# Optimization experiments

Hardware: AMD Instinct MI355X
Metric: run time of the kernel (lower is better)

The kernel has to match this reference:

```python
import jax, jax.numpy as jnp
import numpy as np

BLOCK = 8
INDICES_RADIUS = 127.0  # radius of int8 index dtype


def _dct_matrix(n: int) -> np.ndarray:
    """Orthonormal DCT-II matrix M[element, frequency] matching transforms.cosine."""
    e = np.arange(n)[:, None].astype(np.float64)
    f = np.arange(n)[None, :].astype(np.float64)
    m = np.sqrt(2.0 / n) * np.cos(np.pi * (2.0 * e + 1.0) * f / (2.0 * n))
    m[:, 0] = np.sqrt(1.0 / n)
    return m.astype(np.float32)


def setup_inputs() -> dict:
    key = jax.random.key(0)
    x = jax.random.normal(key, (8192, 8192), dtype=jnp.float32)
    dct = jnp.asarray(_dct_matrix(BLOCK))
    return {"x": x, "dct": dct}


def reference(x, dct):
    # Block splitting: blocked[b1,b2,e1,e2] = x[8*b1+e1, 8*b2+e2]
    H, W = x.shape  # already multiples of BLOCK, so padding is a no-op
    b1, b2 = H // BLOCK, W // BLOCK
    blocked = x.reshape(b1, BLOCK, b2, BLOCK).transpose(0, 2, 1, 3)  # (b1,b2,8,8)
    # Separable blockwise DCT: contract intra-block axes with M[element,freq]
    coeffs = jnp.einsum("bcef,eg,fh->bcgh", blocked, dct, dct)
    # mask is all-ones 8x8 -> row-major flatten of intra-block coefficients
    flat = coeffs.reshape(b1, b2, BLOCK * BLOCK)  # (b1,b2,64)
    # bin(): per-block inf-norm then uniform quantization to int8 bins
    biggest = jnp.max(jnp.abs(flat), axis=-1)  # (b1,b2)
    indices = jnp.round(flat * (INDICES_RADIUS / biggest[..., None])).astype(jnp.int8)
    return indices, biggest
```

## Files before the change

### kernel.cpp

```cpp
#include <hip/hip_runtime.h>


#define IMG_H 8192
#define IMG_W 8192
#define NB1 (IMG_H / 8)
#define NB2 (IMG_W / 8)
#define LSTR 68

__global__ __launch_bounds__(256, 4) void dct_quant_kernel(
    const float* __restrict__ x,
    float* __restrict__ out_idx,
    float* __restrict__ out_big)
{
    constexpr float k1 = 0.4903926402016152f;
    constexpr float k2 = 0.4619397662556434f;
    constexpr float k3 = 0.4157348061512726f;
    constexpr float k4 = 0.35355339059327373f;
    constexpr float k5 = 0.2777851165098011f;
    constexpr float k6 = 0.1913417161825449f;
    constexpr float k7 = 0.0975451610080642f;
    constexpr float M[8][8] = {
        { k4,  k1,  k2,  k3,  k4,  k5,  k6,  k7},
        { k4,  k3,  k6, -k7, -k4, -k1, -k2, -k5},
        { k4,  k5, -k6, -k1, -k4,  k7,  k2,  k3},
        { k4,  k7, -k2, -k5,  k4,  k3, -k6, -k1},
        { k4, -k7, -k2,  k5,  k4, -k3, -k6,  k1},
        { k4, -k5, -k6,  k1, -k4, -k7,  k2, -k3},
        { k4, -k3,  k6,  k7, -k4,  k1, -k2,  k5},
        { k4, -k1,  k2, -k3,  k4, -k5,  k6, -k7},
    };

    __shared__ float t1[64 * LSTR];

    const int t   = threadIdx.x;
    const int tb1 = blockIdx.x >> 7;
    const int tb2 = blockIdx.x & 127;

    const float* tile = x + (size_t)tb1 * 64 * IMG_W + (size_t)tb2 * 64;

    {
        const int r0 = t >> 3;
        const int c0 = t & 7;

        const float4* p0 = (const float4*)(tile + (size_t)r0 * IMG_W + c0 * 8);
        const float4* p1 = (const float4*)(tile + (size_t)(r0 + 32) * IMG_W + c0 * 8);
        const float4 a0 = p0[0];
        const float4 a1 = p0[1];
        const float4 b0 = p1[0];
        const float4 b1 = p1[1];

        {
            const float u[8] = {a0.x, a0.y, a0.z, a0.w, a1.x, a1.y, a1.z, a1.w};
            float w[8];
#pragma unroll
            for (int h = 0; h < 8; ++h) {
                float s = u[0] * M[0][h];
#pragma unroll
                for (int f = 1; f < 8; ++f) s = fmaf(u[f], M[f][h], s);
                w[h] = s;
            }
            float* d = &t1[r0 * LSTR + c0 * 8];
            ((float4*)d)[0] = make_float4(w[0], w[1], w[2], w[3]);
            ((float4*)d)[1] = make_float4(w[4], w[5], w[6], w[7]);
        }
        {
            const float u[8] = {b0.x, b0.y, b0.z, b0.w, b1.x, b1.y, b1.z, b1.w};
            float w[8];
#pragma unroll
            for (int h = 0; h < 8; ++h) {
                float s = u[0] * M[0][h];
#pragma unroll
                for (int f = 1; f < 8; ++f) s = fmaf(u[f], M[f][h], s);
                w[h] = s;
            }
            float* d = &t1[(r0 + 32) * LSTR + c0 * 8];
            ((float4*)d)[0] = make_float4(w[0], w[1], w[2], w[3]);
            ((float4*)d)[1] = make_float4(w[4], w[5], w[6], w[7]);
        }
    }
    __syncthreads();

#pragma unroll
    for (int k = 0; k < 2; ++k) {
        const int s   = t + k * 256;
        const int bb  = s >> 3;
        const int h   = s & 7;
        const int bbr = bb >> 3;
        const int bbc = bb & 7;

        const float* col = &t1[bbr * 8 * LSTR + bbc * 8 + h];
        float v[8];
#pragma unroll
        for (int e = 0; e < 8; ++e) v[e] = col[e * LSTR];

        float c[8];
        float big = 0.0f;
#pragma unroll
        for (int g = 0; g < 8; ++g) {
            float s2 = M[0][g] * v[0];
#pragma unroll
            for (int e = 1; e < 8; ++e) s2 = fmaf(M[e][g], v[e], s2);
            c[g] = s2;
            big = fmaxf(big, fabsf(s2));
        }
        big = fmaxf(big, __shfl_xor(big, 1));
        big = fmaxf(big, __shfl_xor(big, 2));
        big = fmaxf(big, __shfl_xor(big, 4));

        const float scale = 127.0f / big;
        const int b1 = tb1 * 8 + bbr;
        const int b2 = tb2 * 8 + bbc;
        const size_t blk = (size_t)b1 * NB2 + b2;

        float* o = out_idx + blk * 64 + h;
#pragma unroll
        for (int g = 0; g < 8; ++g) o[g * 8] = rintf(c[g] * scale);
        if (h == 0) out_big[blk] = big;
    }
}

extern "C" void kernel_launch(void* const* d_in, const int* in_sizes, int n_in,
                              void* d_out, int out_size, void* d_ws, size_t ws_size,
                              hipStream_t stream) {
    const float* x = (const float*)d_in[0];
    float* out = (float*)d_out;
    float* out_idx = out;
    float* out_big = out + (size_t)NB1 * NB2 * 64;

    dct_quant_kernel<<<16384, 256, 0, stream>>>(x, out_idx, out_big);
}
```

Before: 442.9 us.

## Replace shared-memory transpose with register shuffles and vectorize output stores

```diff
diff --git a/kernel.cpp b/kernel.cpp
--- a/kernel.cpp
+++ b/kernel.cpp
@@ -5,117 +5,126 @@
 #define IMG_W 8192
 #define NB1 (IMG_H / 8)
 #define NB2 (IMG_W / 8)
-#define LSTR 68
+
+__device__ __constant__ const float kM[8][8] = {
+    { 0.35355339059327373f,  0.4903926402016152f,  0.4619397662556434f,
+      0.4157348061512726f,  0.35355339059327373f,  0.2777851165098011f,
+      0.1913417161825449f,  0.0975451610080642f },
+    { 0.35355339059327373f,  0.4157348061512726f,  0.1913417161825449f,
+     -0.0975451610080642f, -0.35355339059327373f, -0.4903926402016152f,
+     -0.4619397662556434f, -0.2777851165098011f },
+    { 0.35355339059327373f,  0.2777851165098011f, -0.1913417161825449f,
+     -0.4903926402016152f, -0.35355339059327373f,  0.0975451610080642f,
+      0.4619397662556434f,  0.4157348061512726f },
+    { 0.35355339059327373f,  0.0975451610080642f, -0.4619397662556434f,
+     -0.2777851165098011f,  0.35355339059327373f,  0.4157348061512726f,
+     -0.1913417161825449f, -0.4903926402016152f },
+    { 0.35355339059327373f, -0.0975451610080642f, -0.4619397662556434f,
+      0.2777851165098011f,  0.35355339059327373f, -0.4157348061512726f,
+     -0.1913417161825449f,  0.4903926402016152f },
+    { 0.35355339059327373f, -0.2777851165098011f, -0.1913417161825449f,
+      0.4903926402016152f, -0.35355339059327373f, -0.0975451610080642f,
+      0.4619397662556434f, -0.4157348061512726f },
+    { 0.35355339059327373f, -0.4157348061512726f,  0.1913417161825449f,
+      0.0975451610080642f, -0.35355339059327373f,  0.4903926402016152f,
+     -0.4619397662556434f,  0.2777851165098011f },
+    { 0.35355339059327373f, -0.4903926402016152f,  0.4619397662556434f,
+     -0.4157348061512726f,  0.35355339059327373f, -0.2777851165098011f,
+      0.1913417161825449f, -0.0975451610080642f },
+};
+
+__device__ __forceinline__ void transpose8(float c[8], const int j) {
+#pragma unroll
+    for (int m = 1; m <= 4; m <<= 1) {
+        const bool hi = (j & m) != 0;
+#pragma unroll
+        for (int g = 0; g < 8; ++g) {
+            if ((g & m) == 0) {
+                const float a = c[g];
+                const float b = c[g + m];
+                const float send = hi ? a : b;
+                const float recv = __shfl_xor(send, m, 64);
+                c[g]     = hi ? recv : a;
+                c[g + m] = hi ? b : recv;
+            }
+        }
+    }
+}
+
+__device__ __forceinline__ void dct_block(float u[8], const int j,
+                                          float* __restrict__ out_idx,
+                                          float* __restrict__ out_big,
+                                          const size_t blk) {
+    float w[8];
+#pragma unroll
+    for (int h = 0; h < 8; ++h) {
+        float s = u[0] * kM[0][h];
+#pragma unroll
+        for (int f = 1; f < 8; ++f) s = fmaf(u[f], kM[f][h], s);
+        w[h] = s;
+    }
+
+    transpose8(w, j);
+
+    float c[8];
+    float big = 0.0f;
+#pragma unroll
+    for (int g = 0; g < 8; ++g) {
+        float s = kM[0][g] * w[0];
+#pragma unroll
+        for (int e = 1; e < 8; ++e) s = fmaf(kM[e][g], w[e], s);
+        c[g] = s;
+        big = fmaxf(big, fabsf(s));
+    }
+
+    big = fmaxf(big, __shfl_xor(big, 1, 64));
+    big = fmaxf(big, __shfl_xor(big, 2, 64));
+    big = fmaxf(big, __shfl_xor(big, 4, 64));
+
+    const float scale = 127.0f / big;
+#pragma unroll
+    for (int g = 0; g < 8; ++g) c[g] = rintf(c[g] * scale);
+
+    transpose8(c, j);
+
+    float* o = out_idx + blk * 64 + (size_t)j * 8;
+    ((float4*)o)[0] = make_float4(c[0], c[1], c[2], c[3]);
+    ((float4*)o)[1] = make_float4(c[4], c[5], c[6], c[7]);
+    if (j == 0) out_big[blk] = big;
+}
 
 __global__ __launch_bounds__(256, 4) void dct_quant_kernel(
     const float* __restrict__ x,
     float* __restrict__ out_idx,
     float* __restrict__ out_big)
 {
-    constexpr float k1 = 0.4903926402016152f;
-    constexpr float k2 = 0.4619397662556434f;
-    constexpr float k3 = 0.4157348061512726f;
-    constexpr float k4 = 0.35355339059327373f;
-    constexpr float k5 = 0.2777851165098011f;
-    constexpr float k6 = 0.1913417161825449f;
-    constexpr float k7 = 0.0975451610080642f;
-    constexpr float M[8][8] = {
-        { k4,  k1,  k2,  k3,  k4,  k5,  k6,  k7},
-        { k4,  k3,  k6, -k7, -k4, -k1, -k2, -k5},
-        { k4,  k5, -k6, -k1, -k4,  k7,  k2,  k3},
-        { k4,  k7, -k2, -k5,  k4,  k3, -k6, -k1},
-        { k4, -k7, -k2,  k5,  k4, -k3, -k6,  k1},
-        { k4, -k5, -k6,  k1, -k4, -k7,  k2, -k3},
-        { k4, -k3,  k6,  k7, -k4,  k1, -k2,  k5},
-        { k4, -k1,  k2, -k3,  k4, -k5,  k6, -k7},
-    };
-
-    __shared__ float t1[64 * LSTR];
-
     const int t   = threadIdx.x;
     const int tb1 = blockIdx.x >> 7;
     const int tb2 = blockIdx.x & 127;
 
+    const int j    = t & 7;
+    const int bbc  = (t >> 3) & 7;
+    const int bbr0 = t >> 6;
+
     const float* tile = x + (size_t)tb1 * 64 * IMG_W + (size_t)tb2 * 64;
 
+    const float* r0 = tile + (size_t)(bbr0 * 8 + j) * IMG_W + bbc * 8;
+    const float* r1 = r0 + (size_t)32 * IMG_W;
+    const float4 a0 = ((const float4*)r0)[0];
+    const float4 a1 = ((const float4*)r0)[1];
+    const float4 b0 = ((const float4*)r1)[0];
+    const float4 b1 = ((const float4*)r1)[1];
+
+    const int b1_0 = tb1 * 8 + bbr0;
+    const int b2   = tb2 * 8 + bbc;
+
     {
-        const int r0 = t >> 3;
-        const int c0 = t & 7;
-
-        const float4* p0 = (const float4*)(tile + (size_t)r0 * IMG_W + c0 * 8);
-        const float4* p1 = (const float4*)(tile + (size_t)(r0 + 32) * IMG_W + c0 * 8);
-        const float4 a0 = p0[0];
-        const float4 a1 = p0[1];
-        const float4 b0 = p1[0];
-        const float4 b1 = p1[1];
-
-        {
-            const float u[8] = {a0.x, a0.y, a0.z, a0.w, a1.x, a1.y, a1.z, a1.w};
-            float w[8];
-#pragma unroll
-            for (int h = 0; h < 8; ++h) {
-                float s = u[0] * M[0][h];
-#pragma unroll
-                for (int f = 1; f < 8; ++f) s = fmaf(u[f], M[f][h], s);
-                w[h] = s;
-            }
-            float* d = &t1[r0 * LSTR + c0 * 8];
-            ((float4*)d)[0] = make_float4(w[0], w[1], w[2], w[3]);
-            ((float4*)d)[1] = make_float4(w[4], w[5], w[6], w[7]);
-        }
-        {
-            const float u[8] = {b0.x, b0.y, b0.z, b0.w, b1.x, b1.y, b1.z, b1.w};
-            float w[8];
-#pragma unroll
-            for (int h = 0; h < 8; ++h) {
-                float s = u[0] * M[0][h];
-#pragma unroll
-                for (int f = 1; f < 8; ++f) s = fmaf(u[f], M[f][h], s);
-                w[h] = s;
-            }
-            float* d = &t1[(r0 + 32) * LSTR + c0 * 8];
-            ((float4*)d)[0] = make_float4(w[0], w[1], w[2], w[3]);
-            ((float4*)d)[1] = make_float4(w[4], w[5], w[6], w[7]);
-        }
+        float u[8] = {a0.x, a0.y, a0.z, a0.w, a1.x, a1.y, a1.z, a1.w};
+        dct_block(u, j, out_idx, out_big, (size_t)b1_0 * NB2 + b2);
     }
-    __syncthreads();
-
-#pragma unroll
-    for (int k = 0; k < 2; ++k) {
-        const int s   = t + k * 256;
-        const int bb  = s >> 3;
-        const int h   = s & 7;
-        const int bbr = bb >> 3;
-        const int bbc = bb & 7;
-
-        const float* col = &t1[bbr * 8 * LSTR + bbc * 8 + h];
-        float v[8];
-#pragma unroll
-        for (int e = 0; e < 8; ++e) v[e] = col[e * LSTR];
-
-        float c[8];
-        float big = 0.0f;
-#pragma unroll
-        for (int g = 0; g < 8; ++g) {
-            float s2 = M[0][g] * v[0];
-#pragma unroll
-            for (int e = 1; e < 8; ++e) s2 = fmaf(M[e][g], v[e], s2);
-            c[g] = s2;
-            big = fmaxf(big, fabsf(s2));
-        }
-        big = fmaxf(big, __shfl_xor(big, 1));
-        big = fmaxf(big, __shfl_xor(big, 2));
-        big = fmaxf(big, __shfl_xor(big, 4));
-
-        const float scale = 127.0f / big;
-        const int b1 = tb1 * 8 + bbr;
-        const int b2 = tb2 * 8 + bbc;
-        const size_t blk = (size_t)b1 * NB2 + b2;
-
-        float* o = out_idx + blk * 64 + h;
-#pragma unroll
-        for (int g = 0; g < 8; ++g) o[g * 8] = rintf(c[g] * scale);
-        if (h == 0) out_big[blk] = big;
+    {
+        float u[8] = {b0.x, b0.y, b0.z, b0.w, b1.x, b1.y, b1.z, b1.w};
+        dct_block(u, j, out_idx, out_big, (size_t)(b1_0 + 4) * NB2 + b2);
     }
 }
 
```

Measured after the change: 439.6 us. About the same (-0.8%).
